# Optimization experiments

Hardware: AMD Instinct MI355X
Metric: run time of the kernel (lower is better)

## Reference

```python
import jax, jax.numpy as jnp
import numpy as np

N = 100000      # nodes
E = 1600000     # edges (avg degree 16)
G = 64          # graphs in batch
IN_DIM, HID, C2, C3, HEADS, NCLS = 64, 128, 64, 32, 4, 5
EPS = 1e-5
NEG_SLOPE = 0.2


def setup_inputs() -> dict:
    key = jax.random.key(0)
    ks = jax.random.split(key, 32)

    def w(k, fan_in, shape):
        return jax.random.normal(k, shape, dtype=jnp.float32) * (1.0 / np.sqrt(fan_in))

    x = jax.random.normal(ks[0], (N, IN_DIM), dtype=jnp.float32)
    edge_index = jax.random.randint(ks[1], (2, E), 0, N)
    batch = jnp.sort(jax.random.randint(ks[2], (N,), 0, G))

    inp = {"x": x, "edge_index": edge_index, "batch": batch}
    # GCN layers (PyG GCNConv: weight then symmetric-normalized aggregation, bias after)
    inp.update(W1=w(ks[3], IN_DIM, (IN_DIM, HID)), b1=jnp.zeros((HID,), jnp.float32))
    inp.update(W2=w(ks[4], HID, (HID, C2)), b2=jnp.zeros((C2,), jnp.float32))
    inp.update(W3=w(ks[5], C2, (C2, C3)), b3=jnp.zeros((C3,), jnp.float32))
    # BatchNorm (inference: running stats)
    def bn_params(k, d):
        k1, k2, k3 = jax.random.split(k, 3)
        return (1.0 + 0.1 * jax.random.normal(k1, (d,), jnp.float32),
                0.1 * jax.random.normal(k2, (d,), jnp.float32),
                0.1 * jax.random.normal(k3, (d,), jnp.float32),
                jax.random.uniform(k, (d,), jnp.float32, 0.5, 1.5))
    inp["g1"], inp["be1"], inp["m1"], inp["v1"] = bn_params(ks[6], HID)
    inp["g2"], inp["be2"], inp["m2"], inp["v2"] = bn_params(ks[7], C2)
    inp["g3"], inp["be3"], inp["m3"], inp["v3"] = bn_params(ks[8], C3)
    # GAT (heads=4, out=32, concat=False -> mean over heads)
    inp["Wg"] = w(ks[9], C3, (C3, HEADS * C3))
    inp["ag_s"] = w(ks[10], C3, (HEADS, C3))
    inp["ag_d"] = w(ks[11], C3, (HEADS, C3))
    inp["bg"] = jnp.zeros((C3,), jnp.float32)
    # classifier MLP 32 -> 16 -> 5
    inp["Wc1"] = w(ks[12], C3, (C3, 16)); inp["bc1"] = jnp.zeros((16,), jnp.float32)
    inp["Wc2"] = w(ks[13], 16, (16, NCLS)); inp["bc2"] = jnp.zeros((NCLS,), jnp.float32)
    return inp


def _bn(h, g, be, m, v):
    return (h - m) * jax.lax.rsqrt(v + EPS) * g + be


def reference(x, edge_index, batch,
              W1, b1, g1, be1, m1, v1,
              W2, b2, g2, be2, m2, v2,
              W3, b3, g3, be3, m3, v3,
              Wg, ag_s, ag_d, bg,
              Wc1, bc1, Wc2, bc2):
    n = x.shape[0]
    loop = jnp.arange(n)
    src = jnp.concatenate([edge_index[0], loop])  # add self-loops (PyG default)
    dst = jnp.concatenate([edge_index[1], loop])

    # GCN symmetric normalization: deg from dst (col), norm = d^-1/2[src]*d^-1/2[dst]
    deg = jnp.zeros((n,), x.dtype).at[dst].add(1.0)
    dinv = jax.lax.rsqrt(deg)  # deg >= 1 due to self-loops
    norm = (dinv[src] * dinv[dst])[:, None]

    def gcn(h, W, b):
        h = h @ W
        return jax.ops.segment_sum(h[src] * norm, dst, num_segments=n) + b

    h = jax.nn.relu(_bn(gcn(x, W1, b1), g1, be1, m1, v1))
    h = jax.nn.relu(_bn(gcn(h, W2, b2), g2, be2, m2, v2))
    h = jax.nn.relu(_bn(gcn(h, W3, b3), g3, be3, m3, v3))

    # GAT: per-edge attention, segment softmax over incoming edges per dst
    hh = (h @ Wg).reshape(n, HEADS, C3)          # [N,H,D]
    a_s = jnp.einsum('nhd,hd->nh', hh, ag_s)     # [N,H]
    a_d = jnp.einsum('nhd,hd->nh', hh, ag_d)
    e = jax.nn.leaky_relu(a_s[src] + a_d[dst], NEG_SLOPE)  # [Eall,H]
    emax = jax.lax.stop_gradient(jax.ops.segment_max(e, dst, num_segments=n))
    ee = jnp.exp(e - emax[dst])
    den = jax.ops.segment_sum(ee, dst, num_segments=n)
    att = ee / den[dst]                          # [Eall,H]
    agg = jax.ops.segment_sum(att[:, :, None] * hh[src], dst, num_segments=n)
    h = jax.nn.relu(agg.mean(axis=1) + bg)       # concat=False -> mean heads

    # global mean pool over graphs
    cnt = jax.ops.segment_sum(jnp.ones((n,), h.dtype), batch, num_segments=G)
    pooled = jax.ops.segment_sum(h, batch, num_segments=G) / jnp.maximum(cnt, 1.0)[:, None]

    # classifier (dropout inactive in eval)
    out = jax.nn.relu(pooled @ Wc1 + bc1) @ Wc2 + bc2
    return out
```

## Files before the change

### kernel.cpp

```cpp
#include <hip/hip_runtime.h>

#define EPSN   1e-5f
#define NEGS   0.2f
#define NGRAPH 64
#define BSHIFT 9
#define NPBK   512
#define GCAP   96

__device__ __forceinline__ float lrelu(float e) { return e > 0.f ? e : NEGS * e; }

__global__ void k_bin_count(const int* __restrict__ ed, int* __restrict__ bsize,
                            int E, int NB) {
    __shared__ int lcnt[1024];
    for (int i = threadIdx.x; i < NB; i += 256) lcnt[i] = 0;
    __syncthreads();
    int chunk = (E + gridDim.x - 1) / gridDim.x;
    int lo = blockIdx.x * chunk;
    int hi = min(E, lo + chunk);
    for (int e = lo + threadIdx.x; e < hi; e += 256)
        atomicAdd(&lcnt[ed[e] >> BSHIFT], 1);
    __syncthreads();
    for (int b = threadIdx.x; b < NB; b += 256)
        if (lcnt[b]) atomicAdd(&bsize[b], lcnt[b]);
}
__global__ void k_bucket_scan(const int* __restrict__ bsize, int* __restrict__ bbase,
                              int* __restrict__ gcur, int NB) {
    int lane = threadIdx.x;
    if (lane >= 64) return;
    int carry = 0;
    int rounds = (NB + 63) / 64;
    for (int r = 0; r < rounds; ++r) {
        int idx = r * 64 + lane;
        int orig = (idx < NB) ? bsize[idx] : 0;
        int v = orig;
#pragma unroll
        for (int o = 1; o < 64; o <<= 1) {
            int t = __shfl_up(v, o, 64);
            if (lane >= o) v += t;
        }
        if (idx < NB) {
            int excl = carry + v - orig;
            bbase[idx] = excl;
            gcur[idx] = excl;
        }
        carry += __shfl(v, 63, 64);
    }
}
__global__ void k_bin_write(const int* __restrict__ es, const int* __restrict__ ed,
                            int* __restrict__ gcur, int2* __restrict__ binned,
                            int E, int NB) {
    __shared__ int lcnt[1024];
    __shared__ int lofs[1024];
    int chunk = (E + gridDim.x - 1) / gridDim.x;
    int lo = blockIdx.x * chunk;
    int hi = min(E, lo + chunk);
    for (int i = threadIdx.x; i < NB; i += 256) lcnt[i] = 0;
    __syncthreads();
    for (int e = lo + threadIdx.x; e < hi; e += 256)
        atomicAdd(&lcnt[ed[e] >> BSHIFT], 1);
    __syncthreads();
    for (int b = threadIdx.x; b < NB; b += 256) {
        int c = lcnt[b];
        lofs[b] = c ? atomicAdd(&gcur[b], c) : 0;
    }
    __syncthreads();
    for (int i = threadIdx.x; i < NB; i += 256) lcnt[i] = 0;
    __syncthreads();
    for (int e = lo + threadIdx.x; e < hi; e += 256) {
        int s = es[e], t = ed[e];
        int b = t >> BSHIFT;
        int pos = lofs[b] + atomicAdd(&lcnt[b], 1);
        binned[pos] = make_int2(s, t);
    }
}
__global__ void k_csr_build(const int2* __restrict__ binned, const int* __restrict__ bbase,
                            const int* __restrict__ bsize, int* __restrict__ rowptr,
                            int* __restrict__ deg, float* __restrict__ dinv,
                            int* __restrict__ csrc, int N) {
    __shared__ int cnt_l[NPBK];
    __shared__ int ofs_l[NPBK];
    int b = blockIdx.x;
    int base = bbase[b];
    int cnt = bsize[b];
    int nlo = b << BSHIFT;
    int nhi = min(N, nlo + NPBK);
    int nv = nhi - nlo;
    int csrbase = base + nlo;
    int tid = threadIdx.x;
    for (int i = tid; i < NPBK; i += 256) cnt_l[i] = (i < nv) ? 1 : 0;
    __syncthreads();
    for (int e = tid; e < cnt; e += 256) {
        int2 st = binned[base + e];
        atomicAdd(&cnt_l[st.y - nlo], 1);
    }
    __syncthreads();
    if (tid < 64) {
        int carry = 0;
#pragma unroll
        for (int r = 0; r < NPBK / 64; ++r) {
            int idx = r * 64 + tid;
            int orig = cnt_l[idx];
            int v = orig;
#pragma unroll
            for (int o = 1; o < 64; o <<= 1) {
                int t = __shfl_up(v, o, 64);
                if (tid >= o) v += t;
            }
            ofs_l[idx] = carry + v - orig;
            carry += __shfl(v, 63, 64);
        }
    }
    __syncthreads();
    for (int i = tid; i < nv; i += 256) {
        int node = nlo + i;
        int d = cnt_l[i];
        rowptr[node] = csrbase + ofs_l[i];
        deg[node] = d;
        dinv[node] = rsqrtf((float)d);
    }
    __syncthreads();
    for (int i = tid; i < NPBK; i += 256) cnt_l[i] = ofs_l[i];
    __syncthreads();
    for (int e = tid; e < cnt; e += 256) {
        int2 st = binned[base + e];
        int p = atomicAdd(&cnt_l[st.y - nlo], 1);
        csrc[csrbase + p] = st.x;
    }
    for (int i = tid; i < nv; i += 256) {
        int p = atomicAdd(&cnt_l[i], 1);
        csrc[csrbase + p] = nlo + i;
    }
}

__global__ void k_scale_x4(const float* __restrict__ x, const float* __restrict__ dinv,
                           float* __restrict__ Xs, int n) {
    int total = n * 16;
    for (int q = blockIdx.x * blockDim.x + threadIdx.x; q < total;
         q += gridDim.x * blockDim.x) {
        float din = dinv[q >> 4];
        float4 xv = ((const float4*)x)[q];
        xv.x *= din; xv.y *= din; xv.z *= din; xv.w *= din;
        ((float4*)Xs)[q] = xv;
    }
}

template <int K, int M, int EPI>
__global__ void k_matmul4(const float* __restrict__ X, const float* __restrict__ W,
                          float* __restrict__ Y, int n,
                          const float* __restrict__ b, const float* __restrict__ g,
                          const float* __restrict__ be, const float* __restrict__ m,
                          const float* __restrict__ v, const float* __restrict__ dinv) {
    __shared__ float Wl[K * M];
    for (int i = threadIdx.x; i < K * M / 4; i += 256)
        ((float4*)Wl)[i] = ((const float4*)W)[i];
    __syncthreads();
    const int TPR = M / 4;
    const int RPB = 256 / TPR;
    const int c4  = (threadIdx.x % TPR) * 4;
    int row = blockIdx.x * RPB + threadIdx.x / TPR;
    if (row >= n) return;
    const float4* xr = (const float4*)(X + (long long)row * K);
    float4 acc = make_float4(0.f, 0.f, 0.f, 0.f);
#pragma unroll
    for (int k4 = 0; k4 < K / 4; ++k4) {
        float4 xv = xr[k4];
        const float* wp = &Wl[(k4 * 4) * M + c4];
        float4 w0 = *(const float4*)(wp);
        float4 w1 = *(const float4*)(wp + M);
        float4 w2 = *(const float4*)(wp + 2 * M);
        float4 w3 = *(const float4*)(wp + 3 * M);
        acc.x += xv.x * w0.x + xv.y * w1.x + xv.z * w2.x + xv.w * w3.x;
        acc.y += xv.x * w0.y + xv.y * w1.y + xv.z * w2.y + xv.w * w3.y;
        acc.z += xv.x * w0.z + xv.y * w1.z + xv.z * w2.z + xv.w * w3.z;
        acc.w += xv.x * w0.w + xv.y * w1.w + xv.z * w2.w + xv.w * w3.w;
    }
    if (EPI == 1) {
        float4 bb = *(const float4*)(b + c4);
        float4 mm = *(const float4*)(m + c4);
        float4 vv = *(const float4*)(v + c4);
        float4 gg = *(const float4*)(g + c4);
        float4 ee = *(const float4*)(be + c4);
        acc.x = fmaxf((acc.x + bb.x - mm.x) * rsqrtf(vv.x + EPSN) * gg.x + ee.x, 0.f);
        acc.y = fmaxf((acc.y + bb.y - mm.y) * rsqrtf(vv.y + EPSN) * gg.y + ee.y, 0.f);
        acc.z = fmaxf((acc.z + bb.z - mm.z) * rsqrtf(vv.z + EPSN) * gg.z + ee.z, 0.f);
        acc.w = fmaxf((acc.w + bb.w - mm.w) * rsqrtf(vv.w + EPSN) * gg.w + ee.w, 0.f);
    } else if (EPI == 2) {
        float din = dinv[row];
        acc.x *= din; acc.y *= din; acc.z *= din; acc.w *= din;
    }
    *(float4*)(Y + (long long)row * M + c4) = acc;
}

template <int M, int EPI>
__global__ void k_agg4(const float* __restrict__ A, const int* __restrict__ rowptr,
                       const int* __restrict__ deg, const int* __restrict__ csrc,
                       const float* __restrict__ dinv,
                       const float* __restrict__ b, const float* __restrict__ g,
                       const float* __restrict__ be, const float* __restrict__ m,
                       const float* __restrict__ v,
                       float* __restrict__ B, int n) {
    const int LPE = M / 4;
    const int EPW = 64 / LPE;
    int node = blockIdx.x * 4 + (threadIdx.x >> 6);
    if (node >= n) return;
    int lane = threadIdx.x & 63;
    int eg = lane / LPE;
    int dl = lane % LPE;
    int beg = rowptr[node];
    int end = beg + deg[node];
    float4 acc = make_float4(0.f, 0.f, 0.f, 0.f);
    for (int base = beg; base < end; base += EPW) {
        int i = base + eg;
        if (i < end) {
            int s = csrc[i];
            float4 xv = *(const float4*)(A + (long long)s * M + dl * 4);
            acc.x += xv.x; acc.y += xv.y; acc.z += xv.z; acc.w += xv.w;
        }
    }
#pragma unroll
    for (int off = LPE; off < 64; off <<= 1) {
        acc.x += __shfl_xor(acc.x, off);
        acc.y += __shfl_xor(acc.y, off);
        acc.z += __shfl_xor(acc.z, off);
        acc.w += __shfl_xor(acc.w, off);
    }
    if (eg == 0) {
        float din = dinv[node];
        acc.x *= din; acc.y *= din; acc.z *= din; acc.w *= din;
        if (EPI == 1) {
            int d0 = dl * 4;
            float4 bb = *(const float4*)(b + d0);
            float4 mm = *(const float4*)(m + d0);
            float4 vv = *(const float4*)(v + d0);
            float4 gg = *(const float4*)(g + d0);
            float4 ee = *(const float4*)(be + d0);
            acc.x = fmaxf((acc.x + bb.x - mm.x) * rsqrtf(vv.x + EPSN) * gg.x + ee.x, 0.f);
            acc.y = fmaxf((acc.y + bb.y - mm.y) * rsqrtf(vv.y + EPSN) * gg.y + ee.y, 0.f);
            acc.z = fmaxf((acc.z + bb.z - mm.z) * rsqrtf(vv.z + EPSN) * gg.z + ee.z, 0.f);
            acc.w = fmaxf((acc.w + bb.w - mm.w) * rsqrtf(vv.w + EPSN) * gg.w + ee.w, 0.f);
        }
        *(float4*)(B + (long long)node * M + dl * 4) = acc;
    }
}

__global__ void k_att2(const float* __restrict__ H3, const float* __restrict__ Wg,
                       const float* __restrict__ ags, const float* __restrict__ agd,
                       float* __restrict__ a_s, float* __restrict__ a_d, int n) {
    __shared__ float Ws[32 * 4], Wd[32 * 4];
    for (int j = threadIdx.x; j < 128; j += 256) {
        int k = j >> 2, h = j & 3;
        float ss = 0.f, dd = 0.f;
        for (int d2 = 0; d2 < 32; ++d2) {
            float w = Wg[k * 128 + h * 32 + d2];
            ss += w * ags[h * 32 + d2];
            dd += w * agd[h * 32 + d2];
        }
        Ws[j] = ss; Wd[j] = dd;
    }
    __syncthreads();
    int total = n * 4;
    for (int i = blockIdx.x * blockDim.x + threadIdx.x; i < total;
         i += gridDim.x * blockDim.x) {
        int ni = i >> 2, h = i & 3;
        const float* hr = H3 + (long long)ni * 32;
        float xs = 0.f, xd = 0.f;
#pragma unroll
        for (int k = 0; k < 32; ++k) {
            float x = hr[k];
            xs += x * Ws[k * 4 + h];
            xd += x * Wd[k * 4 + h];
        }
        a_s[i] = xs;
        a_d[i] = xd;
    }
}

__global__ void k_gat3(const float* __restrict__ H3, const float* __restrict__ a_s,
                       const float* __restrict__ a_d, const int* __restrict__ rowptr,
                       const int* __restrict__ deg, const int* __restrict__ csrc,
                       const float* __restrict__ Wg, const float* __restrict__ bg,
                       float* __restrict__ H4, int n) {
    __shared__ float sc[4][4][GCAP];
    __shared__ int   srcb[4][GCAP];
    __shared__ float2 mi[4][4];
    __shared__ float wb[4][128];
    int w = threadIdx.x >> 6;
    int node = blockIdx.x * 4 + w;
    int lane = threadIdx.x & 63;
    int beg = 0, cnt = 0;
    bool fits = false;
    if (node < n) {
        beg = rowptr[node];
        cnt = deg[node];
        fits = (cnt <= GCAP);
        int hh = lane & 3;
        int slot = lane >> 2;
        float ad = a_d[node * 4 + hh];
        float mx = -1e30f;
        if (fits) {
            for (int i = slot; i < cnt; i += 16) {
                int s = csrc[beg + i];
                if (hh == 0) srcb[w][i] = s;
                float e = lrelu(a_s[s * 4 + hh] + ad);
                sc[w][hh][i] = e;
                mx = fmaxf(mx, e);
            }
        } else {
            for (int i = slot; i < cnt; i += 16)
                mx = fmaxf(mx, lrelu(a_s[csrc[beg + i] * 4 + hh] + ad));
        }
        mx = fmaxf(mx, __shfl_xor(mx, 4));
        mx = fmaxf(mx, __shfl_xor(mx, 8));
        mx = fmaxf(mx, __shfl_xor(mx, 16));
        mx = fmaxf(mx, __shfl_xor(mx, 32));
        float sum = 0.f;
        if (fits) {
            for (int i = slot; i < cnt; i += 16) {
                float p = __expf(sc[w][hh][i] - mx);
                sc[w][hh][i] = p;
                sum += p;
            }
        } else {
            for (int i = slot; i < cnt; i += 16)
                sum += __expf(lrelu(a_s[csrc[beg + i] * 4 + hh] + ad) - mx);
        }
        sum += __shfl_xor(sum, 4);
        sum += __shfl_xor(sum, 8);
        sum += __shfl_xor(sum, 16);
        sum += __shfl_xor(sum, 32);
        if (slot == 0) mi[w][hh] = make_float2(mx, 0.25f / sum);
    }
    __syncthreads();
    int d = lane & 31;
    int h0 = lane >> 5;
    int h2 = h0 + 2;
    float a0 = 0.f, a1 = 0.f;
    if (node < n) {
        float inv0 = mi[w][h0].y;
        float inv2 = mi[w][h2].y;
        if (fits) {
            int i = 0;
            for (; i + 2 <= cnt; i += 2) {
                int s0 = srcb[w][i], s1 = srcb[w][i + 1];
                float x0 = H3[(long long)s0 * 32 + d];
                float x1 = H3[(long long)s1 * 32 + d];
                float w00 = sc[w][h0][i] * inv0,     w01 = sc[w][h2][i] * inv2;
                float w10 = sc[w][h0][i + 1] * inv0, w11 = sc[w][h2][i + 1] * inv2;
                a0 += w00 * x0 + w10 * x1;
                a1 += w01 * x0 + w11 * x1;
            }
            for (; i < cnt; ++i) {
                int s = srcb[w][i];
                float x = H3[(long long)s * 32 + d];
                a0 += sc[w][h0][i] * inv0 * x;
                a1 += sc[w][h2][i] * inv2 * x;
            }
        } else {
            float mx0 = mi[w][h0].x, mx2 = mi[w][h2].x;
            float ad0 = a_d[node * 4 + h0];
            float ad2 = a_d[node * 4 + h2];
            for (int i = 0; i < cnt; ++i) {
                int s = csrc[beg + i];
                float x = H3[(long long)s * 32 + d];
                float w0 = __expf(lrelu(a_s[s * 4 + h0] + ad0) - mx0) * inv0;
                float w1 = __expf(lrelu(a_s[s * 4 + h2] + ad2) - mx2) * inv2;
                a0 += w0 * x;
                a1 += w1 * x;
            }
        }
    }
    wb[w][lane] = a0;
    wb[w][64 + lane] = a1;
    __syncthreads();
    if (node < n) {
        int half = (lane >> 5) * 64;
        float o = 0.f;
#pragma unroll
        for (int j = 0; j < 64; ++j) {
            int jj = half + j;
            o += wb[w][jj] * Wg[(jj & 31) * 128 + (jj >> 5) * 32 + d];
        }
        o += __shfl_xor(o, 32);
        if (lane < 32)
            H4[(long long)node * 32 + d] = fmaxf(o + bg[d], 0.f);
    }
}

__global__ void k_pool_init(float* __restrict__ pooled, float* __restrict__ cnt) {
    int i = blockIdx.x * blockDim.x + threadIdx.x;
    if (i < NGRAPH * 32) pooled[i] = 0.f;
    if (i < NGRAPH) cnt[i] = 0.f;
}
__global__ void k_pool2(const float* __restrict__ h, const int* __restrict__ batch,
                        float* __restrict__ pooled, float* __restrict__ cnt, int n) {
    __shared__ float lp[NGRAPH * 32];
    __shared__ float lc[NGRAPH];
    int tid = threadIdx.x;
    for (int i = tid; i < NGRAPH * 32; i += 256) lp[i] = 0.f;
    for (int i = tid; i < NGRAPH; i += 256) lc[i] = 0.f;
    __syncthreads();
    int per = (n + gridDim.x - 1) / gridDim.x;
    int lo = blockIdx.x * per;
    int hi = min(n, lo + per);
    for (long long i = (long long)lo * 32 + tid; i < (long long)hi * 32; i += 256) {
        int ni = (int)(i >> 5), dd = (int)(i & 31);
        int b = batch[ni];
        atomicAdd(&lp[b * 32 + dd], h[i]);
        if (dd == 0) atomicAdd(&lc[b], 1.f);
    }
    __syncthreads();
    for (int i = tid; i < NGRAPH * 32; i += 256)
        if (lp[i] != 0.f) atomicAdd(&pooled[i], lp[i]);
    for (int i = tid; i < NGRAPH; i += 256)
        if (lc[i] != 0.f) atomicAdd(&cnt[i], lc[i]);
}

__global__ void k_classifier(const float* __restrict__ pooled, const float* __restrict__ cnt,
                             const float* __restrict__ Wc1, const float* __restrict__ bc1,
                             const float* __restrict__ Wc2, const float* __restrict__ bc2,
                             float* __restrict__ out) {
    __shared__ float pl[NGRAPH * 32];
    __shared__ float t1[NGRAPH * 16];
    int tid = threadIdx.x;
    for (int i = tid; i < NGRAPH * 32; i += blockDim.x) {
        int g = i >> 5;
        pl[i] = pooled[i] / fmaxf(cnt[g], 1.f);
    }
    __syncthreads();
    for (int i = tid; i < NGRAPH * 16; i += blockDim.x) {
        int g = i >> 4, c = i & 15;
        float acc = bc1[c];
#pragma unroll
        for (int d = 0; d < 32; ++d) acc += pl[g * 32 + d] * Wc1[d * 16 + c];
        t1[i] = fmaxf(acc, 0.f);
    }
    __syncthreads();
    for (int i = tid; i < NGRAPH * 5; i += blockDim.x) {
        int g = i / 5, c = i % 5;
        float acc = bc2[c];
#pragma unroll
        for (int k = 0; k < 16; ++k) acc += t1[g * 16 + k] * Wc2[k * 5 + c];
        out[i] = acc;
    }
}

static inline dim3 gsz(long long work, int block = 256) {
    long long g = (work + block - 1) / block;
    if (g > 262144) g = 262144;
    if (g < 1) g = 1;
    return dim3((unsigned)g);
}

extern "C" void kernel_launch(void* const* d_in, const int* in_sizes, int n_in,
                              void* d_out, int out_size, void* d_ws, size_t ws_size,
                              hipStream_t stream) {
    const float* x     = (const float*)d_in[0];
    const int*   ei    = (const int*)d_in[1];
    const int*   batch = (const int*)d_in[2];
    const float* W1 = (const float*)d_in[3];  const float* b1 = (const float*)d_in[4];
    const float* W2 = (const float*)d_in[5];  const float* b2 = (const float*)d_in[6];
    const float* W3 = (const float*)d_in[7];  const float* b3 = (const float*)d_in[8];
    const float* g1 = (const float*)d_in[9];  const float* be1 = (const float*)d_in[10];
    const float* m1 = (const float*)d_in[11]; const float* v1  = (const float*)d_in[12];
    const float* g2 = (const float*)d_in[13]; const float* be2 = (const float*)d_in[14];
    const float* m2 = (const float*)d_in[15]; const float* v2  = (const float*)d_in[16];
    const float* g3 = (const float*)d_in[17]; const float* be3 = (const float*)d_in[18];
    const float* m3 = (const float*)d_in[19]; const float* v3  = (const float*)d_in[20];
    const float* Wg  = (const float*)d_in[21];
    const float* ags = (const float*)d_in[22];
    const float* agd = (const float*)d_in[23];
    const float* bg  = (const float*)d_in[24];
    const float* Wc1 = (const float*)d_in[25]; const float* bc1 = (const float*)d_in[26];
    const float* Wc2 = (const float*)d_in[27]; const float* bc2 = (const float*)d_in[28];
    float* out = (float*)d_out;

    const int N = in_sizes[0] / 64;
    const int E = in_sizes[1] / 2;
    const int* esrc = ei;
    const int* edst = ei + E;
    const int NB = (N + NPBK - 1) >> BSHIFT;

    size_t off = 0;
    auto take = [&](size_t bytes) -> void* {
        void* p = (char*)d_ws + off;
        off += bytes;
        off = (off + 255) & ~(size_t)255;
        return p;
    };
    int*   deg    = (int*)take((size_t)N * 4);
    float* dinv   = (float*)take((size_t)N * 4);
    int*   rowptr = (int*)take((size_t)N * 4);
    int*   bsize  = (int*)take((size_t)1024 * 4);
    int*   bbase  = (int*)take((size_t)1024 * 4);
    int*   gcur   = (int*)take((size_t)1024 * 4);
    int*   csrc   = (int*)take((size_t)(E + N) * 4);
    float* bufA   = (float*)take((size_t)N * 64 * 4);
    float* bufB   = (float*)take((size_t)N * 64 * 4);
    float* bufC   = (float*)take((size_t)N * 128 * 4);
    float* a_s    = (float*)take((size_t)N * 4 * 4);
    float* a_d    = (float*)take((size_t)N * 4 * 4);
    float* pooled = (float*)take((size_t)NGRAPH * 32 * 4);
    float* cnt    = (float*)take((size_t)NGRAPH * 4);
    int2*  binned = (int2*)bufC;
    (void)ws_size; (void)n_in; (void)out_size;

    const dim3 B256(256);
    const float* nil = nullptr;

    hipMemsetAsync(bsize, 0, (size_t)NB * 4, stream);
    hipLaunchKernelGGL(k_bin_count, dim3(512), B256, 0, stream, edst, bsize, E, NB);
    hipLaunchKernelGGL(k_bucket_scan, dim3(1), dim3(64), 0, stream, bsize, bbase, gcur, NB);
    hipLaunchKernelGGL(k_bin_write, dim3(512), B256, 0, stream, esrc, edst, gcur, binned, E, NB);
    hipLaunchKernelGGL(k_csr_build, dim3(NB), B256, 0, stream,
                       binned, bbase, bsize, rowptr, deg, dinv, csrc, N);

    hipLaunchKernelGGL(k_scale_x4, gsz((long long)N * 16), B256, 0, stream, x, dinv, bufA, N);
    hipLaunchKernelGGL((k_agg4<64, 0>), dim3((N + 3) / 4), B256, 0, stream,
                       bufA, rowptr, deg, csrc, dinv, nil, nil, nil, nil, nil, bufB, N);
    hipLaunchKernelGGL((k_matmul4<64, 128, 1>), dim3((N + 7) / 8), B256, 0, stream,
                       bufB, W1, bufC, N, b1, g1, be1, m1, v1, nil);
    hipLaunchKernelGGL((k_matmul4<128, 64, 2>), dim3((N + 15) / 16), B256, 0, stream,
                       bufC, W2, bufA, N, nil, nil, nil, nil, nil, dinv);
    hipLaunchKernelGGL((k_agg4<64, 1>), dim3((N + 3) / 4), B256, 0, stream,
                       bufA, rowptr, deg, csrc, dinv, b2, g2, be2, m2, v2, bufB, N);
    hipLaunchKernelGGL((k_matmul4<64, 32, 2>), dim3((N + 31) / 32), B256, 0, stream,
                       bufB, W3, bufA, N, nil, nil, nil, nil, nil, dinv);
    hipLaunchKernelGGL((k_agg4<32, 1>), dim3((N + 3) / 4), B256, 0, stream,
                       bufA, rowptr, deg, csrc, dinv, b3, g3, be3, m3, v3, bufB, N);

    hipLaunchKernelGGL(k_att2, gsz((long long)N * 4), B256, 0, stream,
                       bufB, Wg, ags, agd, a_s, a_d, N);
    hipLaunchKernelGGL(k_gat3, dim3((N + 3) / 4), B256, 0, stream,
                       bufB, a_s, a_d, rowptr, deg, csrc, Wg, bg, bufA, N);

    hipLaunchKernelGGL(k_pool_init, dim3(9), B256, 0, stream, pooled, cnt);
    hipLaunchKernelGGL(k_pool2, dim3(128), B256, 0, stream, bufA, batch, pooled, cnt, N);
    hipLaunchKernelGGL(k_classifier, dim3(1), B256, 0, stream, pooled, cnt, Wc1, bc1, Wc2, bc2, out);
}
```

Before: 694.4 us.

## Fuse input scaling and attention logits into aggregation; restructure GAT kernel

Removes the separate x-scaling kernel by applying dinv[src] inside the first aggregation. It also fuses the attention-logit computation into the layer-3 aggregation epilogue, using a precomputed Wg·a vector and wave shuffles. The GAT kernel now processes all four heads per lane with float4 loads and drops its block-wide syncs. Aggregation loops are unrolled by two to expose more memory parallelism. This saves kernel launches and full passes over N-sized buffers, at the cost of extra dinv gathers per edge and more register pressure.

Measured after the change: 655.1 us. -5.7%, faster.

```diff
diff --git a/kernel.cpp b/kernel.cpp
--- a/kernel.cpp
+++ b/kernel.cpp
@@ -132,18 +132,6 @@
     }
 }
 
-__global__ void k_scale_x4(const float* __restrict__ x, const float* __restrict__ dinv,
-                           float* __restrict__ Xs, int n) {
-    int total = n * 16;
-    for (int q = blockIdx.x * blockDim.x + threadIdx.x; q < total;
-         q += gridDim.x * blockDim.x) {
-        float din = dinv[q >> 4];
-        float4 xv = ((const float4*)x)[q];
-        xv.x *= din; xv.y *= din; xv.z *= din; xv.w *= din;
-        ((float4*)Xs)[q] = xv;
-    }
-}
-
 template <int K, int M, int EPI>
 __global__ void k_matmul4(const float* __restrict__ X, const float* __restrict__ W,
                           float* __restrict__ Y, int n,
@@ -191,7 +179,7 @@
     *(float4*)(Y + (long long)row * M + c4) = acc;
 }
 
-template <int M, int EPI>
+template <int M, int EPI, int PRE>
 __global__ void k_agg4(const float* __restrict__ A, const int* __restrict__ rowptr,
                        const int* __restrict__ deg, const int* __restrict__ csrc,
                        const float* __restrict__ dinv,
@@ -209,13 +197,28 @@
     int beg = rowptr[node];
     int end = beg + deg[node];
     float4 acc = make_float4(0.f, 0.f, 0.f, 0.f);
-    for (int base = beg; base < end; base += EPW) {
-        int i = base + eg;
-        if (i < end) {
-            int s = csrc[i];
-            float4 xv = *(const float4*)(A + (long long)s * M + dl * 4);
-            acc.x += xv.x; acc.y += xv.y; acc.z += xv.z; acc.w += xv.w;
-        }
+    int i = beg + eg;
+    for (; i + EPW < end; i += 2 * EPW) {
+        int s0 = csrc[i];
+        int s1 = csrc[i + EPW];
+        float4 x0 = *(const float4*)(A + (long long)s0 * M + dl * 4);
+        float4 x1 = *(const float4*)(A + (long long)s1 * M + dl * 4);
+        if (PRE) {
+            float w0 = dinv[s0], w1 = dinv[s1];
+            x0.x *= w0; x0.y *= w0; x0.z *= w0; x0.w *= w0;
+            x1.x *= w1; x1.y *= w1; x1.z *= w1; x1.w *= w1;
+        }
+        acc.x += x0.x + x1.x; acc.y += x0.y + x1.y;
+        acc.z += x0.z + x1.z; acc.w += x0.w + x1.w;
+    }
+    if (i < end) {
+        int s = csrc[i];
+        float4 xv = *(const float4*)(A + (long long)s * M + dl * 4);
+        if (PRE) {
+            float w0 = dinv[s];
+            xv.x *= w0; xv.y *= w0; xv.z *= w0; xv.w *= w0;
+        }
+        acc.x += xv.x; acc.y += xv.y; acc.z += xv.z; acc.w += xv.w;
     }
 #pragma unroll
     for (int off = LPE; off < 64; off <<= 1) {
@@ -243,147 +246,226 @@
     }
 }
 
-__global__ void k_att2(const float* __restrict__ H3, const float* __restrict__ Wg,
-                       const float* __restrict__ ags, const float* __restrict__ agd,
-                       float* __restrict__ a_s, float* __restrict__ a_d, int n) {
-    __shared__ float Ws[32 * 4], Wd[32 * 4];
-    for (int j = threadIdx.x; j < 128; j += 256) {
+__global__ void k_wsd(const float* __restrict__ Wg, const float* __restrict__ ags,
+                      const float* __restrict__ agd, float* __restrict__ wsd) {
+    int j = threadIdx.x;
+    if (j < 128) {
         int k = j >> 2, h = j & 3;
         float ss = 0.f, dd = 0.f;
         for (int d2 = 0; d2 < 32; ++d2) {
-            float w = Wg[k * 128 + h * 32 + d2];
-            ss += w * ags[h * 32 + d2];
-            dd += w * agd[h * 32 + d2];
-        }
-        Ws[j] = ss; Wd[j] = dd;
-    }
-    __syncthreads();
-    int total = n * 4;
-    for (int i = blockIdx.x * blockDim.x + threadIdx.x; i < total;
-         i += gridDim.x * blockDim.x) {
-        int ni = i >> 2, h = i & 3;
-        const float* hr = H3 + (long long)ni * 32;
-        float xs = 0.f, xd = 0.f;
-#pragma unroll
-        for (int k = 0; k < 32; ++k) {
-            float x = hr[k];
-            xs += x * Ws[k * 4 + h];
-            xd += x * Wd[k * 4 + h];
-        }
-        a_s[i] = xs;
-        a_d[i] = xd;
-    }
-}
-
-__global__ void k_gat3(const float* __restrict__ H3, const float* __restrict__ a_s,
+            float wv = Wg[k * 128 + h * 32 + d2];
+            ss += wv * ags[h * 32 + d2];
+            dd += wv * agd[h * 32 + d2];
+        }
+        wsd[j] = ss;
+        wsd[128 + j] = dd;
+    }
+}
+
+__global__ void k_agg_att(const float* __restrict__ A, const int* __restrict__ rowptr,
+                          const int* __restrict__ deg, const int* __restrict__ csrc,
+                          const float* __restrict__ dinv,
+                          const float* __restrict__ b, const float* __restrict__ g,
+                          const float* __restrict__ be, const float* __restrict__ m,
+                          const float* __restrict__ v, const float* __restrict__ wsd,
+                          float* __restrict__ H3, float* __restrict__ a_s,
+                          float* __restrict__ a_d, int n) {
+    __shared__ float Wl[256];
+    for (int i = threadIdx.x; i < 256; i += 256) Wl[i] = wsd[i];
+    __syncthreads();
+    const int M = 32, LPE = 8, EPW = 8;
+    int node = blockIdx.x * 4 + (threadIdx.x >> 6);
+    if (node >= n) return;
+    int lane = threadIdx.x & 63;
+    int eg = lane >> 3;
+    int dl = lane & 7;
+    int beg = rowptr[node];
+    int end = beg + deg[node];
+    float4 acc = make_float4(0.f, 0.f, 0.f, 0.f);
+    int i = beg + eg;
+    for (; i + EPW < end; i += 2 * EPW) {
+        int s0 = csrc[i];
+        int s1 = csrc[i + EPW];
+        float4 x0 = *(const float4*)(A + (long long)s0 * M + dl * 4);
+        float4 x1 = *(const float4*)(A + (long long)s1 * M + dl * 4);
+        acc.x += x0.x + x1.x; acc.y += x0.y + x1.y;
+        acc.z += x0.z + x1.z; acc.w += x0.w + x1.w;
+    }
+    if (i < end) {
+        int s = csrc[i];
+        float4 xv = *(const float4*)(A + (long long)s * M + dl * 4);
+        acc.x += xv.x; acc.y += xv.y; acc.z += xv.z; acc.w += xv.w;
+    }
+#pragma unroll
+    for (int off = 8; off < 64; off <<= 1) {
+        acc.x += __shfl_xor(acc.x, off);
+        acc.y += __shfl_xor(acc.y, off);
+        acc.z += __shfl_xor(acc.z, off);
+        acc.w += __shfl_xor(acc.w, off);
+    }
+    float din = dinv[node];
+    int d0 = dl * 4;
+    float4 bb = *(const float4*)(b + d0);
+    float4 mm = *(const float4*)(m + d0);
+    float4 vv = *(const float4*)(v + d0);
+    float4 gg = *(const float4*)(g + d0);
+    float4 ee = *(const float4*)(be + d0);
+    float4 hv;
+    hv.x = fmaxf((acc.x * din + bb.x - mm.x) * rsqrtf(vv.x + EPSN) * gg.x + ee.x, 0.f);
+    hv.y = fmaxf((acc.y * din + bb.y - mm.y) * rsqrtf(vv.y + EPSN) * gg.y + ee.y, 0.f);
+    hv.z = fmaxf((acc.z * din + bb.z - mm.z) * rsqrtf(vv.z + EPSN) * gg.z + ee.z, 0.f);
+    hv.w = fmaxf((acc.w * din + bb.w - mm.w) * rsqrtf(vv.w + EPSN) * gg.w + ee.w, 0.f);
+    if (eg == 0)
+        *(float4*)(H3 + (long long)node * M + d0) = hv;
+    int h = lane & 3, sel = (lane >> 2) & 1;
+    const float* wp = &Wl[sel * 128];
+    float o = 0.f;
+#pragma unroll
+    for (int src = 0; src < 8; ++src) {
+        float bx = __shfl(hv.x, src);
+        float by = __shfl(hv.y, src);
+        float bz = __shfl(hv.z, src);
+        float bw = __shfl(hv.w, src);
+        int k0 = src * 4;
+        o += bx * wp[k0 * 4 + h] + by * wp[(k0 + 1) * 4 + h] +
+             bz * wp[(k0 + 2) * 4 + h] + bw * wp[(k0 + 3) * 4 + h];
+    }
+    if (lane < 4) a_s[node * 4 + h] = o;
+    else if (lane < 8) a_d[node * 4 + h] = o;
+}
+
+__global__ void k_gat4(const float* __restrict__ H3, const float* __restrict__ a_s,
                        const float* __restrict__ a_d, const int* __restrict__ rowptr,
                        const int* __restrict__ deg, const int* __restrict__ csrc,
                        const float* __restrict__ Wg, const float* __restrict__ bg,
                        float* __restrict__ H4, int n) {
-    __shared__ float sc[4][4][GCAP];
+    __shared__ float sc[4][GCAP * 4];
     __shared__ int   srcb[4][GCAP];
-    __shared__ float2 mi[4][4];
     __shared__ float wb[4][128];
     int w = threadIdx.x >> 6;
     int node = blockIdx.x * 4 + w;
+    if (node >= n) return;
     int lane = threadIdx.x & 63;
-    int beg = 0, cnt = 0;
-    bool fits = false;
-    if (node < n) {
-        beg = rowptr[node];
-        cnt = deg[node];
-        fits = (cnt <= GCAP);
-        int hh = lane & 3;
-        int slot = lane >> 2;
-        float ad = a_d[node * 4 + hh];
-        float mx = -1e30f;
-        if (fits) {
-            for (int i = slot; i < cnt; i += 16) {
-                int s = csrc[beg + i];
-                if (hh == 0) srcb[w][i] = s;
-                float e = lrelu(a_s[s * 4 + hh] + ad);
-                sc[w][hh][i] = e;
-                mx = fmaxf(mx, e);
-            }
-        } else {
-            for (int i = slot; i < cnt; i += 16)
-                mx = fmaxf(mx, lrelu(a_s[csrc[beg + i] * 4 + hh] + ad));
-        }
-        mx = fmaxf(mx, __shfl_xor(mx, 4));
-        mx = fmaxf(mx, __shfl_xor(mx, 8));
-        mx = fmaxf(mx, __shfl_xor(mx, 16));
-        mx = fmaxf(mx, __shfl_xor(mx, 32));
-        float sum = 0.f;
-        if (fits) {
-            for (int i = slot; i < cnt; i += 16) {
-                float p = __expf(sc[w][hh][i] - mx);
-                sc[w][hh][i] = p;
-                sum += p;
-            }
-        } else {
-            for (int i = slot; i < cnt; i += 16)
-                sum += __expf(lrelu(a_s[csrc[beg + i] * 4 + hh] + ad) - mx);
-        }
-        sum += __shfl_xor(sum, 4);
-        sum += __shfl_xor(sum, 8);
-        sum += __shfl_xor(sum, 16);
-        sum += __shfl_xor(sum, 32);
-        if (slot == 0) mi[w][hh] = make_float2(mx, 0.25f / sum);
-    }
-    __syncthreads();
+    int beg = rowptr[node];
+    int cnt = deg[node];
+    bool fits = (cnt <= GCAP);
+    float4 ad4 = ((const float4*)a_d)[node];
+    float m0 = -1e30f, m1 = -1e30f, m2 = -1e30f, m3 = -1e30f;
+    if (fits) {
+        for (int e = lane; e < cnt; e += 64) {
+            int s = csrc[beg + e];
+            srcb[w][e] = s;
+            float4 as = ((const float4*)a_s)[s];
+            float e0 = lrelu(as.x + ad4.x);
+            float e1 = lrelu(as.y + ad4.y);
+            float e2 = lrelu(as.z + ad4.z);
+            float e3 = lrelu(as.w + ad4.w);
+            *(float4*)&sc[w][e * 4] = make_float4(e0, e1, e2, e3);
+            m0 = fmaxf(m0, e0); m1 = fmaxf(m1, e1);
+            m2 = fmaxf(m2, e2); m3 = fmaxf(m3, e3);
+        }
+    } else {
+        for (int e = lane; e < cnt; e += 64) {
+            int s = csrc[beg + e];
+            float4 as = ((const float4*)a_s)[s];
+            m0 = fmaxf(m0, lrelu(as.x + ad4.x));
+            m1 = fmaxf(m1, lrelu(as.y + ad4.y));
+            m2 = fmaxf(m2, lrelu(as.z + ad4.z));
+            m3 = fmaxf(m3, lrelu(as.w + ad4.w));
+        }
+    }
+#pragma unroll
+    for (int o = 1; o < 64; o <<= 1) {
+        m0 = fmaxf(m0, __shfl_xor(m0, o));
+        m1 = fmaxf(m1, __shfl_xor(m1, o));
+        m2 = fmaxf(m2, __shfl_xor(m2, o));
+        m3 = fmaxf(m3, __shfl_xor(m3, o));
+    }
+    float s0 = 0.f, s1 = 0.f, s2 = 0.f, s3 = 0.f;
+    if (fits) {
+        for (int e = lane; e < cnt; e += 64) {
+            float4 sv = *(float4*)&sc[w][e * 4];
+            float p0 = __expf(sv.x - m0);
+            float p1 = __expf(sv.y - m1);
+            float p2 = __expf(sv.z - m2);
+            float p3 = __expf(sv.w - m3);
+            *(float4*)&sc[w][e * 4] = make_float4(p0, p1, p2, p3);
+            s0 += p0; s1 += p1; s2 += p2; s3 += p3;
+        }
+    } else {
+        for (int e = lane; e < cnt; e += 64) {
+            int s = csrc[beg + e];
+            float4 as = ((const float4*)a_s)[s];
+            s0 += __expf(lrelu(as.x + ad4.x) - m0);
+            s1 += __expf(lrelu(as.y + ad4.y) - m1);
+            s2 += __expf(lrelu(as.z + ad4.z) - m2);
+            s3 += __expf(lrelu(as.w + ad4.w) - m3);
+        }
+    }
+#pragma unroll
+    for (int o = 1; o < 64; o <<= 1) {
+        s0 += __shfl_xor(s0, o);
+        s1 += __shfl_xor(s1, o);
+        s2 += __shfl_xor(s2, o);
+        s3 += __shfl_xor(s3, o);
+    }
+    float inv0 = 0.25f / s0, inv1 = 0.25f / s1, inv2 = 0.25f / s2, inv3 = 0.25f / s3;
     int d = lane & 31;
     int h0 = lane >> 5;
-    int h2 = h0 + 2;
+    float invA = (h0 == 0) ? inv0 : inv1;
+    float invB = (h0 == 0) ? inv2 : inv3;
     float a0 = 0.f, a1 = 0.f;
-    if (node < n) {
-        float inv0 = mi[w][h0].y;
-        float inv2 = mi[w][h2].y;
-        if (fits) {
-            int i = 0;
-            for (; i + 2 <= cnt; i += 2) {
-                int s0 = srcb[w][i], s1 = srcb[w][i + 1];
-                float x0 = H3[(long long)s0 * 32 + d];
-                float x1 = H3[(long long)s1 * 32 + d];
-                float w00 = sc[w][h0][i] * inv0,     w01 = sc[w][h2][i] * inv2;
-                float w10 = sc[w][h0][i + 1] * inv0, w11 = sc[w][h2][i + 1] * inv2;
-                a0 += w00 * x0 + w10 * x1;
-                a1 += w01 * x0 + w11 * x1;
-            }
-            for (; i < cnt; ++i) {
-                int s = srcb[w][i];
-                float x = H3[(long long)s * 32 + d];
-                a0 += sc[w][h0][i] * inv0 * x;
-                a1 += sc[w][h2][i] * inv2 * x;
-            }
-        } else {
-            float mx0 = mi[w][h0].x, mx2 = mi[w][h2].x;
-            float ad0 = a_d[node * 4 + h0];
-            float ad2 = a_d[node * 4 + h2];
-            for (int i = 0; i < cnt; ++i) {
-                int s = csrc[beg + i];
-                float x = H3[(long long)s * 32 + d];
-                float w0 = __expf(lrelu(a_s[s * 4 + h0] + ad0) - mx0) * inv0;
-                float w1 = __expf(lrelu(a_s[s * 4 + h2] + ad2) - mx2) * inv2;
-                a0 += w0 * x;
-                a1 += w1 * x;
-            }
-        }
+    if (fits) {
+        int i = 0;
+        for (; i + 4 <= cnt; i += 4) {
+            int sA = srcb[w][i],     sB = srcb[w][i + 1];
+            int sC = srcb[w][i + 2], sD = srcb[w][i + 3];
+            float x0 = H3[(long long)sA * 32 + d];
+            float x1 = H3[(long long)sB * 32 + d];
+            float x2 = H3[(long long)sC * 32 + d];
+            float x3 = H3[(long long)sD * 32 + d];
+            float wA0 = sc[w][i * 4 + h0],       wA1 = sc[w][i * 4 + h0 + 2];
+            float wB0 = sc[w][(i + 1) * 4 + h0], wB1 = sc[w][(i + 1) * 4 + h0 + 2];
+            float wC0 = sc[w][(i + 2) * 4 + h0], wC1 = sc[w][(i + 2) * 4 + h0 + 2];
+            float wD0 = sc[w][(i + 3) * 4 + h0], wD1 = sc[w][(i + 3) * 4 + h0 + 2];
+            a0 += wA0 * x0 + wB0 * x1 + wC0 * x2 + wD0 * x3;
+            a1 += wA1 * x0 + wB1 * x1 + wC1 * x2 + wD1 * x3;
+        }
+        for (; i < cnt; ++i) {
+            int s = srcb[w][i];
+            float x = H3[(long long)s * 32 + d];
+            a0 += sc[w][i * 4 + h0] * x;
+            a1 += sc[w][i * 4 + h0 + 2] * x;
+        }
+        a0 *= invA; a1 *= invB;
+    } else {
+        float mA = (h0 == 0) ? m0 : m1;
+        float mB = (h0 == 0) ? m2 : m3;
+        float adA = (h0 == 0) ? ad4.x : ad4.y;
+        float adB = (h0 == 0) ? ad4.z : ad4.w;
+        for (int i = 0; i < cnt; ++i) {
+            int s = csrc[beg + i];
+            float4 as = ((const float4*)a_s)[s];
+            float eA = (h0 == 0) ? (as.x + adA) : (as.y + adA);
+            float eB = (h0 == 0) ? (as.z + adB) : (as.w + adB);
+            float x = H3[(long long)s * 32 + d];
+            a0 += __expf(lrelu(eA) - mA) * x;
+            a1 += __expf(lrelu(eB) - mB) * x;
+        }
+        a0 *= invA; a1 *= invB;
     }
     wb[w][lane] = a0;
     wb[w][64 + lane] = a1;
-    __syncthreads();
-    if (node < n) {
-        int half = (lane >> 5) * 64;
-        float o = 0.f;
-#pragma unroll
-        for (int j = 0; j < 64; ++j) {
-            int jj = half + j;
-            o += wb[w][jj] * Wg[(jj & 31) * 128 + (jj >> 5) * 32 + d];
-        }
-        o += __shfl_xor(o, 32);
-        if (lane < 32)
-            H4[(long long)node * 32 + d] = fmaxf(o + bg[d], 0.f);
-    }
+    int half = h0 * 64;
+    float o = 0.f;
+#pragma unroll
+    for (int j = 0; j < 64; ++j) {
+        int jj = half + j;
+        o += wb[w][jj] * Wg[(jj & 31) * 128 + (jj >> 5) * 32 + d];
+    }
+    o += __shfl_xor(o, 32);
+    if (lane < 32)
+        H4[(long long)node * 32 + d] = fmaxf(o + bg[d], 0.f);
 }
 
 __global__ void k_pool_init(float* __restrict__ pooled, float* __restrict__ cnt) {
@@ -493,6 +575,7 @@
     int*   bsize  = (int*)take((size_t)1024 * 4);
     int*   bbase  = (int*)take((size_t)1024 * 4);
     int*   gcur   = (int*)take((size_t)1024 * 4);
+    float* wsd    = (float*)take((size_t)256 * 4);
     int*   csrc   = (int*)take((size_t)(E + N) * 4);
     float* bufA   = (float*)take((size_t)N * 64 * 4);
     float* bufB   = (float*)take((size_t)N * 64 * 4);
@@ -513,24 +596,23 @@
     hipLaunchKernelGGL(k_bin_write, dim3(512), B256, 0, stream, esrc, edst, gcur, binned, E, NB);
     hipLaunchKernelGGL(k_csr_build, dim3(NB), B256, 0, stream,
                        binned, bbase, bsize, rowptr, deg, dinv, csrc, N);
-
-    hipLaunchKernelGGL(k_scale_x4, gsz((long long)N * 16), B256, 0, stream, x, dinv, bufA, N);
-    hipLaunchKernelGGL((k_agg4<64, 0>), dim3((N + 3) / 4), B256, 0, stream,
-                       bufA, rowptr, deg, csrc, dinv, nil, nil, nil, nil, nil, bufB, N);
+    hipLaunchKernelGGL(k_wsd, dim3(1), dim3(128), 0, stream, Wg, ags, agd, wsd);
+
+    hipLaunchKernelGGL((k_agg4<64, 0, 1>), dim3((N + 3) / 4), B256, 0, stream,
+                       x, rowptr, deg, csrc, dinv, nil, nil, nil, nil, nil, bufB, N);
     hipLaunchKernelGGL((k_matmul4<64, 128, 1>), dim3((N + 7) / 8), B256, 0, stream,
                        bufB, W1, bufC, N, b1, g1, be1, m1, v1, nil);
     hipLaunchKernelGGL((k_matmul4<128, 64, 2>), dim3((N + 15) / 16), B256, 0, stream,
                        bufC, W2, bufA, N, nil, nil, nil, nil, nil, dinv);
-    hipLaunchKernelGGL((k_agg4<64, 1>), dim3((N + 3) / 4), B256, 0, stream,
+    hipLaunchKernelGGL((k_agg4<64, 1, 0>), dim3((N + 3) / 4), B256, 0, stream,
                        bufA, rowptr, deg, csrc, dinv, b2, g2, be2, m2, v2, bufB, N);
     hipLaunchKernelGGL((k_matmul4<64, 32, 2>), dim3((N + 31) / 32), B256, 0, stream,
                        bufB, W3, bufA, N, nil, nil, nil, nil, nil, dinv);
-    hipLaunchKernelGGL((k_agg4<32, 1>), dim3((N + 3) / 4), B256, 0, stream,
-                       bufA, rowptr, deg, csrc, dinv, b3, g3, be3, m3, v3, bufB, N);
-
-    hipLaunchKernelGGL(k_att2, gsz((long long)N * 4), B256, 0, stream,
-                       bufB, Wg, ags, agd, a_s, a_d, N);
-    hipLaunchKernelGGL(k_gat3, dim3((N + 3) / 4), B256, 0, stream,
+    hipLaunchKernelGGL(k_agg_att, dim3((N + 3) / 4), B256, 0, stream,
+                       bufA, rowptr, deg, csrc, dinv, b3, g3, be3, m3, v3,
+                       wsd, bufB, a_s, a_d, N);
+
+    hipLaunchKernelGGL(k_gat4, dim3((N + 3) / 4), B256, 0, stream,
                        bufB, a_s, a_d, rowptr, deg, csrc, Wg, bg, bufA, N);
 
     hipLaunchKernelGGL(k_pool_init, dim3(9), B256, 0, stream, pooled, cnt);
```
